# Optimization experiments

Hardware: AMD Instinct MI355X
Metric: run time of the kernel (lower is better)

The kernel has to match this reference:

```python
import jax, jax.numpy as jnp
import numpy as np

TOP_K = 8


def setup_inputs() -> dict:
    key = jax.random.key(0)
    k1, k2 = jax.random.split(key)
    hidden_states = jax.random.normal(k1, (16384, 2048), dtype=jnp.float32)
    weight = jax.random.normal(k2, (64, 2048), dtype=jnp.float32) * 0.02
    return {"hidden_states": hidden_states, "weight": weight}


def reference(hidden_states, weight):
    # router_logits = F.linear(hidden_states, weight): [T, E]
    router_logits = jnp.einsum('th,eh->te', hidden_states, weight)
    # softmax in float32 as in the original
    router_probs = jax.nn.softmax(router_logits.astype(jnp.float32), axis=-1)
    router_top_values, router_indices = jax.lax.top_k(router_probs, TOP_K)
    # norm_topk_prob=True: renormalize selected probs to sum to 1
    router_top_values = router_top_values / jnp.sum(router_top_values, axis=-1, keepdims=True)
    return (router_logits,
            router_top_values.astype(hidden_states.dtype),
            router_indices)
```

## Files before the change

kernel.cpp:

```cpp
#include <hip/hip_runtime.h>
#include <math.h>

#define T_TOKENS 16384
#define HID      2048
#define NE       64
#define TOPK     8
#define TM       32
#define BK       128
#define NCH      (HID / BK)
#define RSTR     272
#define A_SPL    (32 * RSTR)
#define ABUF     (3 * A_SPL)
#define LDS_BYTES (2 * ABUF)

#define WS_SHORT8 49152

typedef float  f32x4  __attribute__((ext_vector_type(4)));
typedef short  short8 __attribute__((ext_vector_type(8)));

#define MFMA16(A, B, C) __builtin_amdgcn_mfma_f32_16x16x32_bf16((A), (B), (C), 0, 0, 0)

static __device__ __forceinline__ unsigned short f2bf(float x) {
    unsigned u = __builtin_bit_cast(unsigned, x);
    return (unsigned short)((u + 0x7FFFu + ((u >> 16) & 1u)) >> 16);
}
static __device__ __forceinline__ float bf2f(unsigned short h) {
    unsigned u = ((unsigned)h) << 16;
    return __builtin_bit_cast(float, u);
}
static __device__ __forceinline__ void split1(float x, unsigned short& h0,
                                              unsigned short& h1, unsigned short& h2) {
    h0 = f2bf(x); float r = x - bf2f(h0);
    h1 = f2bf(r); r = r - bf2f(h1);
    h2 = f2bf(r);
}
#define SPLIT4(V, B, S0, S1, S2) do {                                             \
    unsigned short h0_, h1_, h2_;                                                 \
    split1((V).x, h0_, h1_, h2_); (S0)[(B)+0]=(short)h0_; (S1)[(B)+0]=(short)h1_; (S2)[(B)+0]=(short)h2_; \
    split1((V).y, h0_, h1_, h2_); (S0)[(B)+1]=(short)h0_; (S1)[(B)+1]=(short)h1_; (S2)[(B)+1]=(short)h2_; \
    split1((V).z, h0_, h1_, h2_); (S0)[(B)+2]=(short)h0_; (S1)[(B)+2]=(short)h1_; (S2)[(B)+2]=(short)h2_; \
    split1((V).w, h0_, h1_, h2_); (S0)[(B)+3]=(short)h0_; (S1)[(B)+3]=(short)h1_; (S2)[(B)+3]=(short)h2_; \
} while (0)

__global__ __launch_bounds__(256) void split_weight_kernel(
    const float* __restrict__ weight, short8* __restrict__ ws8)
{
    const int n = blockIdx.x;
    const int o = threadIdx.x;
    const float4 w0 = *(const float4*)&weight[(size_t)n * HID + o * 8];
    const float4 w1 = *(const float4*)&weight[(size_t)n * HID + o * 8 + 4];
    short8 s0, s1, s2;
    SPLIT4(w0, 0, s0, s1, s2);
    SPLIT4(w1, 4, s0, s1, s2);
    const int t    = o >> 2;
    const int lane = (o & 3) * 16 + (n & 15);
    const int e    = n >> 4;
    const int base = t * 256 + e * 64 + lane;
    ws8[base]         = s0;
    ws8[base + 16384] = s1;
    ws8[base + 32768] = s2;
}

__global__ __launch_bounds__(256, 2) void router_kernel(
    const float* __restrict__ hidden,
    const short8* __restrict__ bfrag,
    float* __restrict__ out_logits,
    float* __restrict__ out_vals,
    float* __restrict__ out_idxf)
{
    __shared__ __align__(16) char smem[LDS_BYTES];
    double (*lg)[NE + 1] = reinterpret_cast<double(*)[NE + 1]>(smem);

    const int tid  = threadIdx.x;
    const int tok0 = blockIdx.x * TM;
    const int lane = tid & 63;
    const int wave = tid >> 6;
    const int tw   = wave & 1;
    const int eh   = wave >> 1;

    const int fr = lane & 15;
    const int fk = lane >> 4;

    int rowmap[4], colmap[4];
    {
        const unsigned short mb = f2bf((float)fr);
        const unsigned short ob = f2bf(0.03125f);
        short8 vm, vo;
        #pragma unroll
        for (int j = 0; j < 8; ++j) { vm[j] = (short)mb; vo[j] = (short)ob; }
        const f32x4 z = {0.f, 0.f, 0.f, 0.f};
        const f32x4 pr = MFMA16(vm, vo, z);
        const f32x4 pc = MFMA16(vo, vm, z);
        #pragma unroll
        for (int i = 0; i < 4; ++i) {
            rowmap[i] = (int)(pr[i] + 0.5f);
            colmap[i] = (int)(pc[i] + 0.5f);
        }
    }

    const int ar   = tid >> 3;
    const int ac16 = (tid & 7) * 16;
    const float* aG = hidden + (size_t)(tok0 + ar) * HID + ac16;
    const int aWOff = ar * RSTR + ac16 * 2;

    const short8* bP = bfrag + eh * 128 + lane;

    const int aOff = (tw * 16 + fr) * RSTR + fk * 16;

    const f32x4 z4 = {0.f, 0.f, 0.f, 0.f};
    f32x4 acch0 = z4, acch1 = z4;
    f32x4 accl0 = z4, accl1 = z4;
    double accd0[4] = {0, 0, 0, 0}, accd1[4] = {0, 0, 0, 0};

    float4 pa[4];

    {
        #pragma unroll
        for (int q = 0; q < 4; ++q) pa[q] = *(const float4*)(aG + 4 * q);
        short8 sa0a, sa0b, sa1a, sa1b, sa2a, sa2b;
        SPLIT4(pa[0], 0, sa0a, sa1a, sa2a); SPLIT4(pa[1], 4, sa0a, sa1a, sa2a);
        SPLIT4(pa[2], 0, sa0b, sa1b, sa2b); SPLIT4(pa[3], 4, sa0b, sa1b, sa2b);
        char* aW = smem + aWOff;
        *(short8*)(aW            ) = sa0a;  *(short8*)(aW             + 16) = sa0b;
        *(short8*)(aW +   A_SPL  ) = sa1a;  *(short8*)(aW +   A_SPL   + 16) = sa1b;
        *(short8*)(aW + 2*A_SPL  ) = sa2a;  *(short8*)(aW + 2*A_SPL   + 16) = sa2b;
    }
    __syncthreads();

    for (int c = 0; c < NCH; ++c) {
        const int cur = c & 1;
        const char* bufc = smem + cur * ABUF;

        if (c + 1 < NCH) {
            const int off = (c + 1) * BK;
            #pragma unroll
            for (int q = 0; q < 4; ++q) pa[q] = *(const float4*)(aG + off + 4 * q);
        }

        #pragma unroll
        for (int st = 0; st < 4; ++st) {
            const int t  = c * 4 + st;
            const int ao = aOff + st * 64;
            const short8 A0 = *(const short8*)(bufc + ao);
            const short8 A1 = *(const short8*)(bufc + A_SPL + ao);
            const short8 A2 = *(const short8*)(bufc + 2 * A_SPL + ao);
            const short8 B00 = bP[t * 256];
            const short8 B01 = bP[t * 256 + 64];
            const short8 B10 = bP[t * 256 + 16384];
            const short8 B11 = bP[t * 256 + 16384 + 64];
            const short8 B20 = bP[t * 256 + 32768];
            const short8 B21 = bP[t * 256 + 32768 + 64];
            acch0 = MFMA16(A0, B00, acch0);  acch1 = MFMA16(A0, B01, acch1);
            accl0 = MFMA16(A0, B10, accl0);  accl1 = MFMA16(A0, B11, accl1);
            accl0 = MFMA16(A1, B00, accl0);  accl1 = MFMA16(A1, B01, accl1);
            accl0 = MFMA16(A1, B10, accl0);  accl1 = MFMA16(A1, B11, accl1);
            accl0 = MFMA16(A0, B20, accl0);  accl1 = MFMA16(A0, B21, accl1);
            accl0 = MFMA16(A2, B00, accl0);  accl1 = MFMA16(A2, B01, accl1);
        }

        #pragma unroll
        for (int i = 0; i < 4; ++i) {
            accd0[i] += (double)acch0[i];
            accd1[i] += (double)acch1[i];
        }
        acch0 = z4; acch1 = z4;

        if (c + 1 < NCH) {
            short8 sa0a, sa0b, sa1a, sa1b, sa2a, sa2b;
            SPLIT4(pa[0], 0, sa0a, sa1a, sa2a); SPLIT4(pa[1], 4, sa0a, sa1a, sa2a);
            SPLIT4(pa[2], 0, sa0b, sa1b, sa2b); SPLIT4(pa[3], 4, sa0b, sa1b, sa2b);
            char* aW = smem + (cur ^ 1) * ABUF + aWOff;
            *(short8*)(aW            ) = sa0a;  *(short8*)(aW             + 16) = sa0b;
            *(short8*)(aW +   A_SPL  ) = sa1a;  *(short8*)(aW +   A_SPL   + 16) = sa1b;
            *(short8*)(aW + 2*A_SPL  ) = sa2a;  *(short8*)(aW + 2*A_SPL   + 16) = sa2b;
        }
        __syncthreads();
    }

    #pragma unroll
    for (int i = 0; i < 4; ++i) {
        const int trow = tw * 16 + rowmap[i];
        const int tok  = tok0 + trow;
        const int e0   = eh * 32 + colmap[i];
        const double l0 = accd0[i] + (double)accl0[i];
        const double l1 = accd1[i] + (double)accl1[i];
        out_logits[(size_t)tok * NE + e0]      = (float)l0;
        out_logits[(size_t)tok * NE + e0 + 16] = (float)l1;
        lg[trow][e0]      = l0;
        lg[trow][e0 + 16] = l1;
    }
    __syncthreads();

    for (int tt = wave; tt < TM; tt += 4) {
        double cur = lg[tt][lane];
        double first = 0.0;
        float  s = 0.f, myv = 0.f;
        int myi = 0;
        #pragma unroll
        for (int i = 0; i < TOPK; ++i) {
            double mv = cur;
            #pragma unroll
            for (int off = 32; off; off >>= 1) {
                const double ov = __shfl_xor(mv, off);
                mv = ov > mv ? ov : mv;
            }
            const unsigned long long m = __ballot(cur == mv);
            const int mi = __ffsll(m) - 1;
            if (i == 0) first = mv;
            const float e = expf((float)(mv - first));
            s += e;
            if (lane == i)  { myv = e; myi = mi; }
            if (lane == mi) cur = -INFINITY;
        }
        if (lane < TOPK) {
            const int tok = tok0 + tt;
            out_vals[(size_t)tok * TOPK + lane] = myv / s;
            out_idxf[(size_t)tok * TOPK + lane] = (float)myi;
        }
    }
}

extern "C" void kernel_launch(void* const* d_in, const int* in_sizes, int n_in,
                              void* d_out, int out_size, void* d_ws, size_t ws_size,
                              hipStream_t stream) {
    const float* hidden = (const float*)d_in[0];
    const float* weight = (const float*)d_in[1];

    float* out        = (float*)d_out;
    float* out_logits = out;
    float* out_vals   = out + (size_t)T_TOKENS * NE;
    float* out_idxf   = out + (size_t)T_TOKENS * NE + (size_t)T_TOKENS * TOPK;

    short8* ws8 = (short8*)d_ws;

    hipLaunchKernelGGL(split_weight_kernel, dim3(NE), dim3(256), 0, stream,
                       weight, ws8);
    hipLaunchKernelGGL(router_kernel, dim3(T_TOKENS / TM), dim3(256), 0, stream,
                       hidden, (const short8*)ws8, out_logits, out_vals, out_idxf);
}
```

Baseline: 233.2 us.

## Halve token tile, give each wave 16 experts, and use a cheaper bf16 split

The token tile drops from 32 to 16 rows, and each of the four waves now computes all 16 tokens against its own 16-expert slice. Per-thread accumulators and staging registers shrink, so launch bounds are raised to allow 4 blocks per CU. The three-way bf16 split now uses add-and-mask rounding and packs value pairs directly into 32-bit words, replacing per-element round-to-nearest-even conversions. Costs are twice as many weight-fragment reads from cache per token, and slightly different rounding of the split terms, which remains an exact decomposition.

```diff
diff --git a/kernel.cpp b/kernel.cpp
--- a/kernel.cpp
+++ b/kernel.cpp
@@ -5,18 +5,19 @@
 #define HID      2048
 #define NE       64
 #define TOPK     8
-#define TM       32
+#define TM       16
 #define BK       128
 #define NCH      (HID / BK)
 #define RSTR     272
-#define A_SPL    (32 * RSTR)
+#define A_SPL    (TM * RSTR)
 #define ABUF     (3 * A_SPL)
 #define LDS_BYTES (2 * ABUF)
 
 #define WS_SHORT8 49152
 
-typedef float  f32x4  __attribute__((ext_vector_type(4)));
-typedef short  short8 __attribute__((ext_vector_type(8)));
+typedef float    f32x4  __attribute__((ext_vector_type(4)));
+typedef short    short8 __attribute__((ext_vector_type(8)));
+typedef unsigned uint4v __attribute__((ext_vector_type(4)));
 
 #define MFMA16(A, B, C) __builtin_amdgcn_mfma_f32_16x16x32_bf16((A), (B), (C), 0, 0, 0)
 
@@ -24,44 +25,53 @@
     unsigned u = __builtin_bit_cast(unsigned, x);
     return (unsigned short)((u + 0x7FFFu + ((u >> 16) & 1u)) >> 16);
 }
-static __device__ __forceinline__ float bf2f(unsigned short h) {
-    unsigned u = ((unsigned)h) << 16;
-    return __builtin_bit_cast(float, u);
-}
-static __device__ __forceinline__ void split1(float x, unsigned short& h0,
-                                              unsigned short& h1, unsigned short& h2) {
-    h0 = f2bf(x); float r = x - bf2f(h0);
-    h1 = f2bf(r); r = r - bf2f(h1);
-    h2 = f2bf(r);
-}
-#define SPLIT4(V, B, S0, S1, S2) do {                                             \
-    unsigned short h0_, h1_, h2_;                                                 \
-    split1((V).x, h0_, h1_, h2_); (S0)[(B)+0]=(short)h0_; (S1)[(B)+0]=(short)h1_; (S2)[(B)+0]=(short)h2_; \
-    split1((V).y, h0_, h1_, h2_); (S0)[(B)+1]=(short)h0_; (S1)[(B)+1]=(short)h1_; (S2)[(B)+1]=(short)h2_; \
-    split1((V).z, h0_, h1_, h2_); (S0)[(B)+2]=(short)h0_; (S1)[(B)+2]=(short)h1_; (S2)[(B)+2]=(short)h2_; \
-    split1((V).w, h0_, h1_, h2_); (S0)[(B)+3]=(short)h0_; (S1)[(B)+3]=(short)h1_; (S2)[(B)+3]=(short)h2_; \
-} while (0)
+
+static __device__ __forceinline__ void split8(const float4 v0, const float4 v1,
+                                              uint4v& p0, uint4v& p1, uint4v& p2)
+{
+    const float x[8] = {v0.x, v0.y, v0.z, v0.w, v1.x, v1.y, v1.z, v1.w};
+    #pragma unroll
+    for (int j = 0; j < 4; ++j) {
+        const float xe = x[2 * j], xo = x[2 * j + 1];
+        const unsigned ue  = __builtin_bit_cast(unsigned, xe);
+        const unsigned m0e = (ue + 0x8000u) & 0xFFFF0000u;
+        const float    r1e = xe - __builtin_bit_cast(float, m0e);
+        const unsigned u1e = __builtin_bit_cast(unsigned, r1e);
+        const unsigned m1e = (u1e + 0x8000u) & 0xFFFF0000u;
+        const float    r2e = r1e - __builtin_bit_cast(float, m1e);
+        const unsigned u2e = __builtin_bit_cast(unsigned, r2e);
+        const unsigned uo  = __builtin_bit_cast(unsigned, xo);
+        const unsigned m0o = (uo + 0x8000u) & 0xFFFF0000u;
+        const float    r1o = xo - __builtin_bit_cast(float, m0o);
+        const unsigned u1o = __builtin_bit_cast(unsigned, r1o);
+        const unsigned m1o = (u1o + 0x8000u) & 0xFFFF0000u;
+        const float    r2o = r1o - __builtin_bit_cast(float, m1o);
+        const unsigned u2o = __builtin_bit_cast(unsigned, r2o);
+        p0[j] = m0o | (m0e >> 16);
+        p1[j] = m1o | (m1e >> 16);
+        p2[j] = (u2o & 0xFFFF0000u) | (u2e >> 16);
+    }
+}
 
 __global__ __launch_bounds__(256) void split_weight_kernel(
-    const float* __restrict__ weight, short8* __restrict__ ws8)
+    const float* __restrict__ weight, uint4v* __restrict__ ws)
 {
     const int n = blockIdx.x;
     const int o = threadIdx.x;
     const float4 w0 = *(const float4*)&weight[(size_t)n * HID + o * 8];
     const float4 w1 = *(const float4*)&weight[(size_t)n * HID + o * 8 + 4];
-    short8 s0, s1, s2;
-    SPLIT4(w0, 0, s0, s1, s2);
-    SPLIT4(w1, 4, s0, s1, s2);
+    uint4v p0, p1, p2;
+    split8(w0, w1, p0, p1, p2);
     const int t    = o >> 2;
     const int lane = (o & 3) * 16 + (n & 15);
     const int e    = n >> 4;
     const int base = t * 256 + e * 64 + lane;
-    ws8[base]         = s0;
-    ws8[base + 16384] = s1;
-    ws8[base + 32768] = s2;
-}
-
-__global__ __launch_bounds__(256, 2) void router_kernel(
+    ws[base]         = p0;
+    ws[base + 16384] = p1;
+    ws[base + 32768] = p2;
+}
+
+__global__ __launch_bounds__(256, 4) void router_kernel(
     const float* __restrict__ hidden,
     const short8* __restrict__ bfrag,
     float* __restrict__ out_logits,
@@ -75,8 +85,6 @@
     const int tok0 = blockIdx.x * TM;
     const int lane = tid & 63;
     const int wave = tid >> 6;
-    const int tw   = wave & 1;
-    const int eh   = wave >> 1;
 
     const int fr = lane & 15;
     const int fk = lane >> 4;
@@ -98,32 +106,31 @@
         }
     }
 
-    const int ar   = tid >> 3;
-    const int ac16 = (tid & 7) * 16;
-    const float* aG = hidden + (size_t)(tok0 + ar) * HID + ac16;
-    const int aWOff = ar * RSTR + ac16 * 2;
-
-    const short8* bP = bfrag + eh * 128 + lane;
-
-    const int aOff = (tw * 16 + fr) * RSTR + fk * 16;
+    const int ar  = tid >> 4;
+    const int ac8 = (tid & 15) * 8;
+    const float* aG = hidden + (size_t)(tok0 + ar) * HID + ac8;
+    const int aWOff = ar * RSTR + ac8 * 2;
+
+    const short8* bP = bfrag + wave * 64 + lane;
+
+    const int aOff = fr * RSTR + fk * 16;
 
     const f32x4 z4 = {0.f, 0.f, 0.f, 0.f};
-    f32x4 acch0 = z4, acch1 = z4;
-    f32x4 accl0 = z4, accl1 = z4;
-    double accd0[4] = {0, 0, 0, 0}, accd1[4] = {0, 0, 0, 0};
-
-    float4 pa[4];
+    f32x4 acch = z4;
+    f32x4 accl = z4;
+    double accd[4] = {0, 0, 0, 0};
+
+    float4 pa0, pa1;
 
     {
-        #pragma unroll
-        for (int q = 0; q < 4; ++q) pa[q] = *(const float4*)(aG + 4 * q);
-        short8 sa0a, sa0b, sa1a, sa1b, sa2a, sa2b;
-        SPLIT4(pa[0], 0, sa0a, sa1a, sa2a); SPLIT4(pa[1], 4, sa0a, sa1a, sa2a);
-        SPLIT4(pa[2], 0, sa0b, sa1b, sa2b); SPLIT4(pa[3], 4, sa0b, sa1b, sa2b);
+        pa0 = *(const float4*)(aG);
+        pa1 = *(const float4*)(aG + 4);
+        uint4v p0, p1, p2;
+        split8(pa0, pa1, p0, p1, p2);
         char* aW = smem + aWOff;
-        *(short8*)(aW            ) = sa0a;  *(short8*)(aW             + 16) = sa0b;
-        *(short8*)(aW +   A_SPL  ) = sa1a;  *(short8*)(aW +   A_SPL   + 16) = sa1b;
-        *(short8*)(aW + 2*A_SPL  ) = sa2a;  *(short8*)(aW + 2*A_SPL   + 16) = sa2b;
+        *(uint4v*)(aW            ) = p0;
+        *(uint4v*)(aW +   A_SPL  ) = p1;
+        *(uint4v*)(aW + 2*A_SPL  ) = p2;
     }
     __syncthreads();
 
@@ -133,8 +140,8 @@
 
         if (c + 1 < NCH) {
             const int off = (c + 1) * BK;
-            #pragma unroll
-            for (int q = 0; q < 4; ++q) pa[q] = *(const float4*)(aG + off + 4 * q);
+            pa0 = *(const float4*)(aG + off);
+            pa1 = *(const float4*)(aG + off + 4);
         }
 
         #pragma unroll
@@ -144,50 +151,40 @@
             const short8 A0 = *(const short8*)(bufc + ao);
             const short8 A1 = *(const short8*)(bufc + A_SPL + ao);
             const short8 A2 = *(const short8*)(bufc + 2 * A_SPL + ao);
-            const short8 B00 = bP[t * 256];
-            const short8 B01 = bP[t * 256 + 64];
-            const short8 B10 = bP[t * 256 + 16384];
-            const short8 B11 = bP[t * 256 + 16384 + 64];
-            const short8 B20 = bP[t * 256 + 32768];
-            const short8 B21 = bP[t * 256 + 32768 + 64];
-            acch0 = MFMA16(A0, B00, acch0);  acch1 = MFMA16(A0, B01, acch1);
-            accl0 = MFMA16(A0, B10, accl0);  accl1 = MFMA16(A0, B11, accl1);
-            accl0 = MFMA16(A1, B00, accl0);  accl1 = MFMA16(A1, B01, accl1);
-            accl0 = MFMA16(A1, B10, accl0);  accl1 = MFMA16(A1, B11, accl1);
-            accl0 = MFMA16(A0, B20, accl0);  accl1 = MFMA16(A0, B21, accl1);
-            accl0 = MFMA16(A2, B00, accl0);  accl1 = MFMA16(A2, B01, accl1);
-        }
-
-        #pragma unroll
-        for (int i = 0; i < 4; ++i) {
-            accd0[i] += (double)acch0[i];
-            accd1[i] += (double)acch1[i];
-        }
-        acch0 = z4; acch1 = z4;
+            const short8 B0 = bP[t * 256];
+            const short8 B1 = bP[t * 256 + 16384];
+            const short8 B2 = bP[t * 256 + 32768];
+            acch = MFMA16(A0, B0, acch);
+            accl = MFMA16(A0, B1, accl);
+            accl = MFMA16(A1, B0, accl);
+            accl = MFMA16(A1, B1, accl);
+            accl = MFMA16(A0, B2, accl);
+            accl = MFMA16(A2, B0, accl);
+        }
+
+        #pragma unroll
+        for (int i = 0; i < 4; ++i) accd[i] += (double)acch[i];
+        acch = z4;
 
         if (c + 1 < NCH) {
-            short8 sa0a, sa0b, sa1a, sa1b, sa2a, sa2b;
-            SPLIT4(pa[0], 0, sa0a, sa1a, sa2a); SPLIT4(pa[1], 4, sa0a, sa1a, sa2a);
-            SPLIT4(pa[2], 0, sa0b, sa1b, sa2b); SPLIT4(pa[3], 4, sa0b, sa1b, sa2b);
+            uint4v p0, p1, p2;
+            split8(pa0, pa1, p0, p1, p2);
             char* aW = smem + (cur ^ 1) * ABUF + aWOff;
-            *(short8*)(aW            ) = sa0a;  *(short8*)(aW             + 16) = sa0b;
-            *(short8*)(aW +   A_SPL  ) = sa1a;  *(short8*)(aW +   A_SPL   + 16) = sa1b;
-            *(short8*)(aW + 2*A_SPL  ) = sa2a;  *(short8*)(aW + 2*A_SPL   + 16) = sa2b;
+            *(uint4v*)(aW            ) = p0;
+            *(uint4v*)(aW +   A_SPL  ) = p1;
+            *(uint4v*)(aW + 2*A_SPL  ) = p2;
         }
         __syncthreads();
     }
 
     #pragma unroll
     for (int i = 0; i < 4; ++i) {
-        const int trow = tw * 16 + rowmap[i];
+        const int trow = rowmap[i];
         const int tok  = tok0 + trow;
-        const int e0   = eh * 32 + colmap[i];
-        const double l0 = accd0[i] + (double)accl0[i];
-        const double l1 = accd1[i] + (double)accl1[i];
-        out_logits[(size_t)tok * NE + e0]      = (float)l0;
-        out_logits[(size_t)tok * NE + e0 + 16] = (float)l1;
-        lg[trow][e0]      = l0;
-        lg[trow][e0 + 16] = l1;
+        const int e0   = wave * 16 + colmap[i];
+        const double l0 = accd[i] + (double)accl[i];
+        out_logits[(size_t)tok * NE + e0] = (float)l0;
+        lg[trow][e0] = l0;
     }
     __syncthreads();
 
@@ -231,10 +228,10 @@
     float* out_vals   = out + (size_t)T_TOKENS * NE;
     float* out_idxf   = out + (size_t)T_TOKENS * NE + (size_t)T_TOKENS * TOPK;
 
-    short8* ws8 = (short8*)d_ws;
+    uint4v* ws = (uint4v*)d_ws;
 
     hipLaunchKernelGGL(split_weight_kernel, dim3(NE), dim3(256), 0, stream,
-                       weight, ws8);
+                       weight, ws);
     hipLaunchKernelGGL(router_kernel, dim3(T_TOKENS / TM), dim3(256), 0, stream,
-                       hidden, (const short8*)ws8, out_logits, out_vals, out_idxf);
-}
+                       hidden, (const short8*)ws, out_logits, out_vals, out_idxf);
+}
```

Result: no change. 229.9 us (-1.4%).
